# Optimization experiments

Measured on AMD Instinct MI355X. Metric: run time of the kernel, lower is better.

Reference implementation:

```python
import jax, jax.numpy as jnp
import numpy as np

B = 32          # batch_size
S = 64          # num_subgraph
D = 8           # dim_multi_hot (module-level global in source repo)
NE = S * D      # num_edges = 512
NNODES = 1024
E = 150000      # incidence rows
IN_UNITS = [16, 32, 32]
OUT_UNITS = [32, 32, 16]


def _glorot(key, shape):
    # glorot_normal over last two dims (out, in)
    fan_out, fan_in = shape[-2], shape[-1]
    std = (2.0 / (fan_in + fan_out)) ** 0.5
    return std * jax.random.normal(key, shape, dtype=jnp.float32)


def setup_inputs() -> dict:
    key = jax.random.key(0)
    ks = jax.random.split(key, 10)
    nodes_features = jax.random.normal(ks[0], (NNODES * S, IN_UNITS[0]), dtype=jnp.float32)
    c0 = jax.random.randint(ks[1], (E,), 0, B, dtype=jnp.int32)
    c1 = jax.random.randint(ks[2], (E,), 0, NNODES, dtype=jnp.int32)
    c2 = jax.random.randint(ks[3], (E,), 0, S, dtype=jnp.int32)
    c3 = jax.random.randint(ks[4], (E,), 0, D, dtype=jnp.int32)
    incidence_matrix = jnp.stack([c0, c1, c2, c3], axis=1)
    return {
        'nodes_features': nodes_features,
        'in_core0': _glorot(ks[5], (NE, IN_UNITS[1], IN_UNITS[0])),
        'in_bias0': jnp.zeros((NE, IN_UNITS[1], 1), jnp.float32),
        'in_core1': _glorot(ks[6], (NE, IN_UNITS[2], IN_UNITS[1])),
        'in_bias1': jnp.zeros((NE, IN_UNITS[2], 1), jnp.float32),
        'out_core0': _glorot(ks[7], (NE, OUT_UNITS[1], OUT_UNITS[0])),
        'out_bias0': jnp.zeros((NE, OUT_UNITS[1], 1), jnp.float32),
        'out_core1': _glorot(ks[8], (NE, OUT_UNITS[2], OUT_UNITS[1])),
        'out_bias1': jnp.zeros((NE, OUT_UNITS[2], 1), jnp.float32),
        'incidence_matrix': incidence_matrix,
    }


def reference(nodes_features, in_core0, in_bias0, in_core1, in_bias1,
              out_core0, out_bias0, out_core1, out_bias1, incidence_matrix):
    c0 = incidence_matrix[:, 0]
    c1 = incidence_matrix[:, 1]
    c2 = incidence_matrix[:, 2]
    c3 = incidence_matrix[:, 3]

    # gather node features per incidence row: [E, in0]
    x = nodes_features[c1 * S + c2]
    eidx = c2 * D + c3  # per-edge weight index, < NE

    # per-edge MLP (gathered batched matmul + bias + relu)
    for W, b in ((in_core0, in_bias0), (in_core1, in_bias1)):
        x = jax.nn.relu(jnp.einsum('eoi,ei->eo', W[eidx], x) + b[eidx, :, 0])

    # unsorted segment mean over irregular edge groups
    seg = c0 * (D * S) + c2 * D + c3
    nseg = B * S * D
    sums = jax.ops.segment_sum(x, seg, num_segments=nseg)           # [B*NE, 32]
    cnt = jax.ops.segment_sum(jnp.ones((x.shape[0], 1), x.dtype), seg, num_segments=nseg)
    ef = jnp.where(cnt > 0, sums / jnp.maximum(cnt, 1.0), 0.0)       # [B*NE, 32]

    # output MLP: weights tiled over batch (einsum avoids explicit repeat)
    ef = ef.reshape(B, NE, -1)
    for W, b in ((out_core0, out_bias0), (out_core1, out_bias1)):
        ef = jax.nn.relu(jnp.einsum('eoi,bei->beo', W, ef) + b[None, :, :, 0])

    return ef.reshape(B * NE, OUT_UNITS[-1], 1)
```

## Files before the change

kernel.cpp:

```cpp
#include <hip/hip_runtime.h>

#define B_    32
#define S_    64
#define D_    8
#define NE_   512
#define E_    150000
#define CAP   512

#define SCAT_BLK  1024
#define SCAT_R    4
#define SCAT_EPB  (SCAT_BLK*SCAT_R)
#define SCAT_NB   ((E_ + SCAT_EPB - 1)/SCAT_EPB)


__global__ void zero_cursor(int* __restrict__ cursor) {
    cursor[threadIdx.x] = 0;
}

__global__ __launch_bounds__(SCAT_BLK)
void scatter_kernel(const int* __restrict__ inc,
                    int* __restrict__ cursor,
                    int* __restrict__ payload) {
    __shared__ int lcount[NE_];
    __shared__ int lbase[NE_];
    __shared__ int stash_p[SCAT_EPB];
    __shared__ int stash_m[SCAT_EPB];
    const int tid = threadIdx.x;

    for (int i = tid; i < NE_; i += SCAT_BLK) lcount[i] = 0;
    __syncthreads();

    #pragma unroll
    for (int r = 0; r < SCAT_R; ++r) {
        const int e = blockIdx.x * SCAT_EPB + r * SCAT_BLK + tid;
        int m = -1, p = 0;
        if (e < E_) {
            const int4 c = ((const int4*)inc)[e];
            const int eidx = c.z * D_ + c.w;
            const int lpos = atomicAdd(&lcount[eidx], 1);
            m = (eidx << 16) | lpos;
            p = (c.x << 16) | (c.y * S_ + c.z);
        }
        stash_m[r * SCAT_BLK + tid] = m;
        stash_p[r * SCAT_BLK + tid] = p;
    }
    __syncthreads();

    for (int i = tid; i < NE_; i += SCAT_BLK) {
        const int c = lcount[i];
        lbase[i] = (c > 0) ? atomicAdd(&cursor[i], c) : 0;
    }
    __syncthreads();

    #pragma unroll
    for (int r = 0; r < SCAT_R; ++r) {
        const int m = stash_m[r * SCAT_BLK + tid];
        if (m >= 0) {
            const int eidx = m >> 16;
            const int idx  = lbase[eidx] + (m & 0xFFFF);
            if (idx < CAP) payload[eidx * CAP + idx] = stash_p[r * SCAT_BLK + tid];
        }
    }
}

__global__ __launch_bounds__(256)
void main_kernel(const float* __restrict__ nf,
                 const float* __restrict__ iw0, const float* __restrict__ ib0,
                 const float* __restrict__ iw1, const float* __restrict__ ib1,
                 const float* __restrict__ ow0, const float* __restrict__ ob0,
                 const float* __restrict__ ow1, const float* __restrict__ ob1,
                 const int* __restrict__ cursor, const int* __restrict__ payload,
                 float* __restrict__ out) {
    const int eidx = blockIdx.x;
    const int tid  = threadIdx.x;

    __shared__ float acc[32][33];
    __shared__ float hb[32][33];
    __shared__ float cnts[32];
    __shared__ __align__(16) float q0s[1024];
    __shared__ __align__(16) float q1s[512];
    __shared__ float qb0s[32], qb1s[16];

    const float* __restrict__ w0  = iw0 + (size_t)eidx * 512;
    const float* __restrict__ bb0 = ib0 + (size_t)eidx * 32;
    const float* __restrict__ w1  = iw1 + (size_t)eidx * 1024;
    const float* __restrict__ bb1 = ib1 + (size_t)eidx * 32;

    for (int i = tid; i < 1024; i += 256) q0s[i] = ow0[(size_t)eidx * 1024 + i];
    for (int i = tid; i < 512;  i += 256) q1s[i] = ow1[(size_t)eidx * 512 + i];
    if (tid < 32) { qb0s[tid] = ob0[(size_t)eidx * 32 + tid]; cnts[tid] = 0.f; }
    else if (tid < 48) qb1s[tid - 32] = ob1[(size_t)eidx * 16 + (tid - 32)];
    for (int i = tid; i < 32 * 33; i += 256) ((float*)acc)[i] = 0.f;
    __syncthreads();

    const int n = min(cursor[eidx], CAP);
    for (int i = tid; i < n; i += 256) {
        const int p   = payload[eidx * CAP + i];
        const int b   = p >> 16;
        const int row = p & 0xFFFF;

        float x[16];
        {
            const float4* xp = (const float4*)(nf + (size_t)row * 16);
            #pragma unroll
            for (int k = 0; k < 4; ++k) {
                float4 v = xp[k];
                x[4*k] = v.x; x[4*k+1] = v.y; x[4*k+2] = v.z; x[4*k+3] = v.w;
            }
        }
        float h[32];
        #pragma unroll 4
        for (int o = 0; o < 32; ++o) {
            float a = bb0[o];
            #pragma unroll
            for (int k = 0; k < 16; ++k) a = fmaf(w0[o * 16 + k], x[k], a);
            h[o] = fmaxf(a, 0.f);
        }
        float h2[32];
        #pragma unroll 4
        for (int o = 0; o < 32; ++o) {
            float a = bb1[o];
            #pragma unroll
            for (int k = 0; k < 32; ++k) a = fmaf(w1[o * 32 + k], h[k], a);
            h2[o] = fmaxf(a, 0.f);
        }
        #pragma unroll
        for (int o = 0; o < 32; ++o) atomicAdd(&acc[b][o], h2[o]);
        atomicAdd(&cnts[b], 1.f);
    }
    __syncthreads();

    {
        const int b  = tid >> 3;
        const int o0 = (tid & 7) * 4;
        const float cv  = cnts[b];
        const float inv = cv > 0.f ? 1.0f / cv : 0.0f;
        #pragma unroll
        for (int j = 0; j < 4; ++j) {
            const int o = o0 + j;
            float d = 0.f;
            #pragma unroll
            for (int k = 0; k < 32; ++k) d = fmaf(q0s[o * 32 + k], acc[b][k], d);
            hb[b][o] = fmaxf(fmaf(d, inv, qb0s[o]), 0.f);
        }
    }
    __syncthreads();

    {
        const int b  = tid >> 3;
        const int o0 = (tid & 7) * 2;
        float r[2];
        #pragma unroll
        for (int j = 0; j < 2; ++j) {
            const int o = o0 + j;
            float d = qb1s[o];
            #pragma unroll
            for (int k = 0; k < 32; ++k) d = fmaf(q1s[o * 32 + k], hb[b][k], d);
            r[j] = fmaxf(d, 0.f);
        }
        float2* op = (float2*)(out + ((size_t)b * NE_ + eidx) * 16 + o0);
        *op = make_float2(r[0], r[1]);
    }
}

extern "C" void kernel_launch(void* const* d_in, const int* in_sizes, int n_in,
                              void* d_out, int out_size, void* d_ws, size_t ws_size,
                              hipStream_t stream) {
    const float* nf  = (const float*)d_in[0];
    const float* iw0 = (const float*)d_in[1];
    const float* ib0 = (const float*)d_in[2];
    const float* iw1 = (const float*)d_in[3];
    const float* ib1 = (const float*)d_in[4];
    const float* ow0 = (const float*)d_in[5];
    const float* ob0 = (const float*)d_in[6];
    const float* ow1 = (const float*)d_in[7];
    const float* ob1 = (const float*)d_in[8];
    const int*   inc = (const int*)d_in[9];

    int* cursor  = (int*)d_ws;
    int* payload = cursor + NE_;

    zero_cursor<<<1, NE_, 0, stream>>>(cursor);
    scatter_kernel<<<SCAT_NB, SCAT_BLK, 0, stream>>>(inc, cursor, payload);
    main_kernel<<<NE_, 256, 0, stream>>>(nf, iw0, ib0, iw1, ib1,
                                         ow0, ob0, ow1, ob1,
                                         cursor, payload, (float*)d_out);
}
```

Before: 145.7 us.

## Fuse zero, scatter, and main kernels into one cooperative kernel; map lanes to outputs

Replaces the three launches (cursor zero, bucket scatter, per-edge MLP) with a single cooperative kernel of 512 blocks that uses grid.sync between phases. Each block buckets a chunk of about 293 incidence rows before computing its own edge's MLP. The per-edge MLP is also restructured so each lane owns one output unit and holds its weight row in registers. Hidden activations are exchanged through LDS with wave barriers, and there is one LDS atomic per lane instead of 32 per thread. This removes launch overhead and the redundant per-thread weight reads, at the cost of grid-wide sync latency and fewer rows processed concurrently per block.

Result: slower. 256.1 us (+75.8%).

```diff
diff --git a/kernel.cpp b/kernel.cpp
--- a/kernel.cpp
+++ b/kernel.cpp
@@ -1,4 +1,6 @@
 #include <hip/hip_runtime.h>
+#include <hip/hip_cooperative_groups.h>
+namespace cg = cooperative_groups;
 
 #define B_    32
 #define S_    64
@@ -6,74 +8,26 @@
 #define NE_   512
 #define E_    150000
 #define CAP   512
-
-#define SCAT_BLK  1024
-#define SCAT_R    4
-#define SCAT_EPB  (SCAT_BLK*SCAT_R)
-#define SCAT_NB   ((E_ + SCAT_EPB - 1)/SCAT_EPB)
+#define CHUNK 293
 
 
-__global__ void zero_cursor(int* __restrict__ cursor) {
-    cursor[threadIdx.x] = 0;
-}
+__global__ __launch_bounds__(256, 2)
+void fused_kernel(const float* __restrict__ nf,
+                  const float* __restrict__ iw0, const float* __restrict__ ib0,
+                  const float* __restrict__ iw1, const float* __restrict__ ib1,
+                  const float* __restrict__ ow0, const float* __restrict__ ob0,
+                  const float* __restrict__ ow1, const float* __restrict__ ob1,
+                  const int* __restrict__ inc,
+                  int* __restrict__ cursor, int* __restrict__ payload,
+                  float* __restrict__ out)
+{
+    const int bid = blockIdx.x;
+    const int tid = threadIdx.x;
+    cg::grid_group grid = cg::this_grid();
 
-__global__ __launch_bounds__(SCAT_BLK)
-void scatter_kernel(const int* __restrict__ inc,
-                    int* __restrict__ cursor,
-                    int* __restrict__ payload) {
     __shared__ int lcount[NE_];
     __shared__ int lbase[NE_];
-    __shared__ int stash_p[SCAT_EPB];
-    __shared__ int stash_m[SCAT_EPB];
-    const int tid = threadIdx.x;
-
-    for (int i = tid; i < NE_; i += SCAT_BLK) lcount[i] = 0;
-    __syncthreads();
-
-    #pragma unroll
-    for (int r = 0; r < SCAT_R; ++r) {
-        const int e = blockIdx.x * SCAT_EPB + r * SCAT_BLK + tid;
-        int m = -1, p = 0;
-        if (e < E_) {
-            const int4 c = ((const int4*)inc)[e];
-            const int eidx = c.z * D_ + c.w;
-            const int lpos = atomicAdd(&lcount[eidx], 1);
-            m = (eidx << 16) | lpos;
-            p = (c.x << 16) | (c.y * S_ + c.z);
-        }
-        stash_m[r * SCAT_BLK + tid] = m;
-        stash_p[r * SCAT_BLK + tid] = p;
-    }
-    __syncthreads();
-
-    for (int i = tid; i < NE_; i += SCAT_BLK) {
-        const int c = lcount[i];
-        lbase[i] = (c > 0) ? atomicAdd(&cursor[i], c) : 0;
-    }
-    __syncthreads();
-
-    #pragma unroll
-    for (int r = 0; r < SCAT_R; ++r) {
-        const int m = stash_m[r * SCAT_BLK + tid];
-        if (m >= 0) {
-            const int eidx = m >> 16;
-            const int idx  = lbase[eidx] + (m & 0xFFFF);
-            if (idx < CAP) payload[eidx * CAP + idx] = stash_p[r * SCAT_BLK + tid];
-        }
-    }
-}
-
-__global__ __launch_bounds__(256)
-void main_kernel(const float* __restrict__ nf,
-                 const float* __restrict__ iw0, const float* __restrict__ ib0,
-                 const float* __restrict__ iw1, const float* __restrict__ ib1,
-                 const float* __restrict__ ow0, const float* __restrict__ ob0,
-                 const float* __restrict__ ow1, const float* __restrict__ ob1,
-                 const int* __restrict__ cursor, const int* __restrict__ payload,
-                 float* __restrict__ out) {
-    const int eidx = blockIdx.x;
-    const int tid  = threadIdx.x;
-
+    __shared__ float hbuf[4][64];
     __shared__ float acc[32][33];
     __shared__ float hb[32][33];
     __shared__ float cnts[32];
@@ -81,52 +35,104 @@
     __shared__ __align__(16) float q1s[512];
     __shared__ float qb0s[32], qb1s[16];
 
-    const float* __restrict__ w0  = iw0 + (size_t)eidx * 512;
-    const float* __restrict__ bb0 = ib0 + (size_t)eidx * 32;
-    const float* __restrict__ w1  = iw1 + (size_t)eidx * 1024;
-    const float* __restrict__ bb1 = ib1 + (size_t)eidx * 32;
+    if (bid < 2) cursor[bid * 256 + tid] = 0;
+    for (int i = tid; i < NE_; i += 256) lcount[i] = 0;
+    __syncthreads();
+    grid.sync();
 
-    for (int i = tid; i < 1024; i += 256) q0s[i] = ow0[(size_t)eidx * 1024 + i];
-    for (int i = tid; i < 512;  i += 256) q1s[i] = ow1[(size_t)eidx * 512 + i];
-    if (tid < 32) { qb0s[tid] = ob0[(size_t)eidx * 32 + tid]; cnts[tid] = 0.f; }
-    else if (tid < 48) qb1s[tid - 32] = ob1[(size_t)eidx * 16 + (tid - 32)];
+    {
+        const int start = bid * CHUNK;
+        const int end   = min(start + CHUNK, E_);
+        int ei0 = -1, lp0 = 0, pl0 = 0;
+        int ei1 = -1, lp1 = 0, pl1 = 0;
+        int e = start + tid;
+        if (e < end) {
+            const int4 c = ((const int4*)inc)[e];
+            ei0 = c.z * D_ + c.w;
+            pl0 = (c.x << 16) | (c.y * S_ + c.z);
+            lp0 = atomicAdd(&lcount[ei0], 1);
+        }
+        e = start + 256 + tid;
+        if (e < end) {
+            const int4 c = ((const int4*)inc)[e];
+            ei1 = c.z * D_ + c.w;
+            pl1 = (c.x << 16) | (c.y * S_ + c.z);
+            lp1 = atomicAdd(&lcount[ei1], 1);
+        }
+        __syncthreads();
+        for (int i = tid; i < NE_; i += 256) {
+            const int c = lcount[i];
+            lbase[i] = (c > 0) ? atomicAdd(&cursor[i], c) : 0;
+        }
+        __syncthreads();
+        if (ei0 >= 0) {
+            const int idx = lbase[ei0] + lp0;
+            if (idx < CAP) payload[ei0 * CAP + idx] = pl0;
+        }
+        if (ei1 >= 0) {
+            const int idx = lbase[ei1] + lp1;
+            if (idx < CAP) payload[ei1 * CAP + idx] = pl1;
+        }
+    }
+    grid.sync();
+
+    const int lane = tid & 63;
+    const int wav  = tid >> 6;
+    const int slot = lane >> 5;
+    const int o    = lane & 31;
+
+    float w0r[16], w1r[32];
+    #pragma unroll
+    for (int j = 0; j < 4; ++j) {
+        float4 v = ((const float4*)(iw0 + (size_t)bid * 512 + o * 16))[j];
+        w0r[4*j] = v.x; w0r[4*j+1] = v.y; w0r[4*j+2] = v.z; w0r[4*j+3] = v.w;
+    }
+    #pragma unroll
+    for (int j = 0; j < 8; ++j) {
+        float4 v = ((const float4*)(iw1 + (size_t)bid * 1024 + o * 32))[j];
+        w1r[4*j] = v.x; w1r[4*j+1] = v.y; w1r[4*j+2] = v.z; w1r[4*j+3] = v.w;
+    }
+    const float b0r = ib0[bid * 32 + o];
+    const float b1r = ib1[bid * 32 + o];
+
+    for (int i = tid; i < 1024; i += 256) q0s[i] = ow0[(size_t)bid * 1024 + i];
+    for (int i = tid; i < 512;  i += 256) q1s[i] = ow1[(size_t)bid * 512 + i];
+    if (tid < 32) { qb0s[tid] = ob0[bid * 32 + tid]; cnts[tid] = 0.f; }
+    else if (tid < 48) qb1s[tid - 32] = ob1[bid * 16 + (tid - 32)];
     for (int i = tid; i < 32 * 33; i += 256) ((float*)acc)[i] = 0.f;
     __syncthreads();
 
-    const int n = min(cursor[eidx], CAP);
-    for (int i = tid; i < n; i += 256) {
-        const int p   = payload[eidx * CAP + i];
+    const int n = min(cursor[bid], CAP);
+    for (int i = wav * 2 + slot; i < n; i += 8) {
+        const int p   = payload[bid * CAP + i];
         const int b   = p >> 16;
         const int row = p & 0xFFFF;
 
         float x[16];
-        {
-            const float4* xp = (const float4*)(nf + (size_t)row * 16);
-            #pragma unroll
-            for (int k = 0; k < 4; ++k) {
-                float4 v = xp[k];
-                x[4*k] = v.x; x[4*k+1] = v.y; x[4*k+2] = v.z; x[4*k+3] = v.w;
-            }
+        #pragma unroll
+        for (int j = 0; j < 4; ++j) {
+            float4 v = ((const float4*)(nf + (size_t)row * 16))[j];
+            x[4*j] = v.x; x[4*j+1] = v.y; x[4*j+2] = v.z; x[4*j+3] = v.w;
         }
-        float h[32];
-        #pragma unroll 4
-        for (int o = 0; o < 32; ++o) {
-            float a = bb0[o];
-            #pragma unroll
-            for (int k = 0; k < 16; ++k) a = fmaf(w0[o * 16 + k], x[k], a);
-            h[o] = fmaxf(a, 0.f);
+        float h = b0r;
+        #pragma unroll
+        for (int k = 0; k < 16; ++k) h = fmaf(w0r[k], x[k], h);
+        h = fmaxf(h, 0.f);
+
+        hbuf[wav][slot * 32 + o] = h;
+        __builtin_amdgcn_wave_barrier();
+        float a = b1r;
+        #pragma unroll
+        for (int j = 0; j < 8; ++j) {
+            float4 v = ((const float4*)&hbuf[wav][slot * 32])[j];
+            a = fmaf(w1r[4*j],   v.x, a); a = fmaf(w1r[4*j+1], v.y, a);
+            a = fmaf(w1r[4*j+2], v.z, a); a = fmaf(w1r[4*j+3], v.w, a);
         }
-        float h2[32];
-        #pragma unroll 4
-        for (int o = 0; o < 32; ++o) {
-            float a = bb1[o];
-            #pragma unroll
-            for (int k = 0; k < 32; ++k) a = fmaf(w1[o * 32 + k], h[k], a);
-            h2[o] = fmaxf(a, 0.f);
-        }
-        #pragma unroll
-        for (int o = 0; o < 32; ++o) atomicAdd(&acc[b][o], h2[o]);
-        atomicAdd(&cnts[b], 1.f);
+        __builtin_amdgcn_wave_barrier();
+        a = fmaxf(a, 0.f);
+
+        atomicAdd(&acc[b][o], a);
+        if (o == 0) atomicAdd(&cnts[b], 1.f);
     }
     __syncthreads();
 
@@ -137,11 +143,11 @@
         const float inv = cv > 0.f ? 1.0f / cv : 0.0f;
         #pragma unroll
         for (int j = 0; j < 4; ++j) {
-            const int o = o0 + j;
+            const int oo = o0 + j;
             float d = 0.f;
             #pragma unroll
-            for (int k = 0; k < 32; ++k) d = fmaf(q0s[o * 32 + k], acc[b][k], d);
-            hb[b][o] = fmaxf(fmaf(d, inv, qb0s[o]), 0.f);
+            for (int k = 0; k < 32; ++k) d = fmaf(q0s[oo * 32 + k], acc[b][k], d);
+            hb[b][oo] = fmaxf(fmaf(d, inv, qb0s[oo]), 0.f);
         }
     }
     __syncthreads();
@@ -152,13 +158,13 @@
         float r[2];
         #pragma unroll
         for (int j = 0; j < 2; ++j) {
-            const int o = o0 + j;
-            float d = qb1s[o];
+            const int oo = o0 + j;
+            float d = qb1s[oo];
             #pragma unroll
-            for (int k = 0; k < 32; ++k) d = fmaf(q1s[o * 32 + k], hb[b][k], d);
+            for (int k = 0; k < 32; ++k) d = fmaf(q1s[oo * 32 + k], hb[b][k], d);
             r[j] = fmaxf(d, 0.f);
         }
-        float2* op = (float2*)(out + ((size_t)b * NE_ + eidx) * 16 + o0);
+        float2* op = (float2*)(out + ((size_t)b * NE_ + bid) * 16 + o0);
         *op = make_float2(r[0], r[1]);
     }
 }
@@ -179,10 +185,10 @@
 
     int* cursor  = (int*)d_ws;
     int* payload = cursor + NE_;
+    float* out   = (float*)d_out;
 
-    zero_cursor<<<1, NE_, 0, stream>>>(cursor);
-    scatter_kernel<<<SCAT_NB, SCAT_BLK, 0, stream>>>(inc, cursor, payload);
-    main_kernel<<<NE_, 256, 0, stream>>>(nf, iw0, ib0, iw1, ib1,
-                                         ow0, ob0, ow1, ob1,
-                                         cursor, payload, (float*)d_out);
+    void* args[] = { &nf, &iw0, &ib0, &iw1, &ib1, &ow0, &ob0, &ow1, &ob1,
+                     &inc, &cursor, &payload, &out };
+    hipLaunchCooperativeKernel((const void*)fused_kernel,
+                               dim3(NE_), dim3(256), args, 0, stream);
 }
```
